# Performance work log

Hardware: AMD Instinct MI355X
Metric: run time of the kernel (lower is better)

Reference implementation:

```python
import jax, jax.numpy as jnp
import numpy as np

D = 128      # flattened state dim (n_dim)
T = 128      # time grid length
N = 32       # quadrature nodes per integral
H = 256      # func MLP hidden
HK = 64      # kernel MLP hidden
ITERS = 3    # IDESolver max_iterations


def setup_inputs() -> dict:
    key = jax.random.key(0)
    ks = jax.random.split(key, 6)
    z0 = jax.random.normal(ks[0], (1, D), jnp.float32)
    t = jnp.linspace(0.0, 1.0, T, dtype=jnp.float32)
    W1 = jax.random.normal(ks[1], (D, H), jnp.float32) / np.float32(np.sqrt(D))
    b1 = jnp.zeros((H,), jnp.float32)
    W2 = jax.random.normal(ks[2], (H, D), jnp.float32) / np.float32(np.sqrt(H))
    b2 = jnp.zeros((D,), jnp.float32)
    Wk1 = jax.random.normal(ks[3], (2, HK), jnp.float32) / np.float32(np.sqrt(2))
    bk1 = jnp.zeros((HK,), jnp.float32)
    # small kernel init keeps the Picard iteration stable
    Wk2 = jax.random.normal(ks[4], (HK, D * D), jnp.float32) * np.float32(0.01 / np.sqrt(HK))
    bk2 = jnp.zeros((D * D,), jnp.float32)
    return dict(z0=z0, t=t, W1=W1, b1=b1, W2=W2, b2=b2,
                Wk1=Wk1, bk1=bk1, Wk2=Wk2, bk2=bk2)


def _spline_coeffs(x, y):
    # natural cubic spline second derivatives M: tridiagonal system, natural BC
    n = x.shape[0]
    h = x[1:] - x[:-1]                       # [T-1]
    A = jnp.zeros((n, n), y.dtype).at[0, 0].set(1.0).at[n - 1, n - 1].set(1.0)
    idx = jnp.arange(1, n - 1)
    A = A.at[idx, idx - 1].set(h[:-1])
    A = A.at[idx, idx].set(2.0 * (h[:-1] + h[1:]))
    A = A.at[idx, idx + 1].set(h[1:])
    slope = (y[1:] - y[:-1]) / h[:, None]
    rhs = jnp.zeros_like(y).at[1:-1].set(6.0 * (slope[1:] - slope[:-1]))
    return jnp.linalg.solve(A, rhs)          # [T, D]


def _spline_eval(x, y, M, q):
    # evaluate spline at flat query points q [Q] -> [Q, D]
    qc = jnp.clip(q, x[0], x[-1])
    i = jnp.clip(jnp.searchsorted(x, qc, side='right') - 1, 0, x.shape[0] - 2)
    h = x[i + 1] - x[i]
    a = (x[i + 1] - qc) / h
    b = (qc - x[i]) / h
    return (a[:, None] * y[i] + b[:, None] * y[i + 1]
            + ((a ** 3 - a)[:, None] * M[i] + (b ** 3 - b)[:, None] * M[i + 1])
            * (h ** 2 / 6.0)[:, None])


def _F(y, W1, b1, W2, b2):
    return jnp.tanh(y @ W1 + b1) @ W2 + b2


def _K(ts, Wk1, bk1, Wk2, bk2):
    # ts [..., 2] -> kernel matrices [..., D, D]
    hden = jnp.tanh(ts @ Wk1 + bk1)
    return (hden @ Wk2 + bk2).reshape(ts.shape[:-1] + (D, D))


def reference(z0, t, W1, b1, W2, b2, Wk1, bk1, Wk2, bk2):
    y0 = z0.reshape(-1)                          # solver state: flattened z0 [D]
    u = jnp.linspace(0.0, 1.0, N, dtype=t.dtype) # unit quad nodes
    wq = jnp.ones((N,), t.dtype).at[0].set(0.5).at[-1].set(0.5)  # trapezoid
    mids = 0.5 * (t[:-1] + t[1:])
    xs = jnp.concatenate([t, mids])              # eval points [P = 2T-1]
    hstep = t[1:] - t[:-1]
    yg = jnp.broadcast_to(y0, (T, D))            # Picard initial guess y^(0)=y0
    for _ in range(ITERS):
        M = _spline_coeffs(t, yg)
        s = xs[:, None] * u[None, :]                              # [P, N], lb=0, ub=x
        ys = _spline_eval(t, yg, M, s.reshape(-1)).reshape(-1, N, D)
        fy = _F(ys, W1, b1, W2, b2)                               # [P, N, D]
        ts = jnp.stack([jnp.broadcast_to(xs[:, None], s.shape), s], -1)
        k = _K(ts, Wk1, bk1, Wk2, bk2)                            # [P, N, D, D]
        integ = jnp.einsum('pnij,pnj->pni', k, fy)
        g = jnp.einsum('pni,n->pi', integ, wq) * (xs / (N - 1))[:, None]  # [P, D]
        g_t, g_m = g[:T], g[T:]
        # Simpson (== RK4 for y-independent RHS) + cumulative integration
        inc = (hstep[:, None] / 6.0) * (g_t[:-1] + 4.0 * g_m + g_t[1:])
        yg = y0[None, :] + jnp.concatenate(
            [jnp.zeros((1, D), yg.dtype), jnp.cumsum(inc, axis=0)])
    return yg[:, None, :]                        # [T, 1, D] like solver.y.unsqueeze(1)
```

## Files before the change

kernel.cpp:

```cpp
#include <hip/hip_runtime.h>
#include <hip/hip_fp16.h>

#define D_  128
#define T_  128
#define P_  255
#define GSZ  32640

#define OFF_YGF   0
#define OFF_COEF  8192
#define OFF_AINV  8704
#define OFF_E     41472
#define OFF_HDW   563712
#define OFF_W1F   828912
#define OFF_W2F   845296
#define OFF_WTT   861680
#define OFF_S     1394160
#define OFF_G2    2459120
#define OFF_CTR   2491760

typedef _Float16 f16;
typedef _Float16 f16x4 __attribute__((ext_vector_type(4)));
typedef float f32x4 __attribute__((ext_vector_type(4)));

__device__ __forceinline__ float tanh_fast(float x) {
  float e = __expf(2.0f * x);
  return 1.0f - 2.0f / (e + 1.0f);
}

__device__ __forceinline__ f16x4 ldfrag(const f16* buf, int row, int kunits,
                                        int kk, int quad) {
  int u = row * kunits + ((kk * 4 + quad) ^ (row & 7));
  return *(const f16x4*)(buf + 4 * u);
}

__global__ __launch_bounds__(256) void k_setup(
    const float* __restrict__ z0, const float* __restrict__ tgrid,
    const float* __restrict__ W1, const float* __restrict__ W2,
    const float* __restrict__ Wk2, const float* __restrict__ bk2,
    __half* __restrict__ ygF, float* __restrict__ coef,
    float* __restrict__ Ainv, __half* __restrict__ W1F,
    __half* __restrict__ W2F, __half* __restrict__ WTC,
    unsigned* __restrict__ ctr) {
  __shared__ __align__(16) unsigned char smem[66560];
  int bid = blockIdx.x, tid = threadIdx.x;
  for (int idx = bid * 256 + tid; idx < 65 * 16384; idx += 256 * 256) {
    int c = idx >> 14, rem = idx & 16383;
    int i = rem >> 7, j = rem & 127;
    float v = (c < 64) ? Wk2[idx] : bk2[rem];
    int kc = c / 5;
    int kr = (c - kc * 5) * 128 + j;
    int kb = kr >> 6, kw = kr & 63;
    WTC[(((kc * 10 + kb) << 7) + i) * 64 + kw] = __float2half(v);
  }
  if (bid == 0) {
    for (int idx = tid; idx < 16384; idx += 256) {
      int l2 = (idx >> 2) & 63, blk = idx >> 8;
      int nt = blk >> 3, rr = l2 & 15;
      ygF[idx] = __float2half(z0[nt * 16 + rr]);
    }
  } else if (bid == 1) {
    for (int idx = tid; idx < 32768; idx += 256) {
      int j = idx & 3, l2 = (idx >> 2) & 63, blk = idx >> 8;
      int nt = blk >> 3, kk = blk & 7, rr = l2 & 15, qd = l2 >> 4;
      int c = nt * 16 + rr, d = kk * 16 + qd * 4 + j;
      W1F[idx] = __float2half(W1[d * 256 + c]);
    }
  } else if (bid == 2) {
    for (int idx = tid; idx < 32768; idx += 256) {
      int j = idx & 3, l2 = (idx >> 2) & 63, blk = idx >> 8;
      int nt = blk >> 4, kk = blk & 15, rr = l2 & 15, qd = l2 >> 4;
      int jcol = nt * 16 + rr, c = kk * 16 + qd * 4 + j;
      W2F[idx] = __float2half(W2[c * 128 + jcol]);
    }
  } else if (bid == 3) {
    if (tid == 0) *ctr = 0u;
  } else if (bid == 255) {
    float* dpL = (float*)smem;
    float* tl  = (float*)(smem + 65024);
    float* cpL = tl + 128;
    float* imL = cpL + 128;
    if (tid < 128) tl[tid] = tgrid[tid];
    __syncthreads();
    if (tid == 0) {
      cpL[0] = 0.0f;
      float cprev = 0.0f;
      for (int i = 1; i <= 126; ++i) {
        float hm = tl[i] - tl[i - 1], hi = tl[i + 1] - tl[i];
        float m = 2.0f * (hm + hi) - hm * cprev;
        float im = 1.0f / m;
        imL[i] = im;
        cprev = hi * im;
        cpL[i] = cprev;
      }
    }
    if (tid < 127) coef[256 + tid] = 1.0f / (tl[tid + 1] - tl[tid]);
    __syncthreads();
    if (tid < 128) {
      int d = tid;
      float dprev = (d == 0) ? 1.0f : 0.0f;
      dpL[d] = dprev;
      for (int i = 1; i <= 126; ++i) {
        float rhs = (i == d) ? 1.0f : 0.0f;
        float hm = tl[i] - tl[i - 1];
        dprev = (rhs - hm * dprev) * imL[i];
        dpL[i * 128 + d] = dprev;
      }
      float x = (d == 127) ? 1.0f : 0.0f;
      Ainv[127 * 128 + d] = x;
      for (int i = 126; i >= 0; --i) {
        x = dpL[i * 128 + d] - cpL[i] * x;
        Ainv[i * 128 + d] = x;
      }
    }
  }
}

__global__ __launch_bounds__(512) void k_fused(
    __half* __restrict__ EF, __half* __restrict__ HDW,
    const __half* __restrict__ ygF,
    const __half* __restrict__ W1F, const __half* __restrict__ W2F,
    const float* __restrict__ b1, const float* __restrict__ b2,
    __half* __restrict__ Sq, float* __restrict__ g,
    const float* __restrict__ tgrid, const float* __restrict__ Wk1,
    const float* __restrict__ bk1, const float* __restrict__ coef,
    const float* __restrict__ Ainv, int it) {
  __shared__ __align__(16) unsigned char smem[32768];
  __shared__ float tl[128], ihL[128];
  __shared__ float sn[32], an[32], bn[32], cA[32], cB[32];
  __shared__ int idn[32];
  f16* RA = (f16*)smem;
  f16* RB = (f16*)(smem + 8192);
  f16* RC = (f16*)(smem + 16384);
  int p = blockIdx.x, tid = threadIdx.x;
  int wv = tid >> 6, l = tid & 63, quad = l >> 4, r = l & 15;

  if (tid < 128) g[p * 128 + tid] = 0.0f;
  if (p == 0) {
    for (int z = tid; z < 8320; z += 512) {
      int kcS = z / 640, kr = z - kcS * 640;
      Sq[kcS * 163840 + 255 * 640 + kr] = __float2half(0.0f);
    }
  }

  if (it == 0) {
    if (tid < 128) tl[tid] = tgrid[tid];
    if (tid < 127) ihL[tid] = coef[256 + tid];
    __syncthreads();
    float xp = (p < T_) ? tl[p] : 0.5f * (tl[p - T_] + tl[p - T_ + 1]);
    if (tid < 32) {
      int n = tid;
      float u = (float)n * (1.0f / 31.0f);
      float q = xp * u;
      float qc = fminf(fmaxf(q, tl[0]), tl[127]);
      int i = (int)floorf(qc * 127.0f);
      i = max(0, min(126, i));
      while (i > 0 && qc < tl[i]) --i;
      while (i < 126 && qc >= tl[i + 1]) ++i;
      float h = tl[i + 1] - tl[i];
      float aa = (tl[i + 1] - qc) / h, bb = (qc - tl[i]) / h;
      sn[n] = q; idn[n] = i; an[n] = aa; bn[n] = bb;
      float h26 = h * h * (1.0f / 6.0f);
      cA[n] = (aa * aa * aa - aa) * h26;
      cB[n] = (bb * bb * bb - bb) * h26;
    }
    __syncthreads();
    #pragma unroll
    for (int pass = 0; pass < 8; ++pass) {
      int n = pass * 4 + (tid >> 7);
      int b = tid & 127;
      int i = idn[n];
      float Gi = 0.0f, Gi1 = 0.0f;
      if (b >= 2) {
        float w = 6.0f * ihL[b - 1];
        Gi  += Ainv[i * 128 + b - 1] * w;
        Gi1 += Ainv[(i + 1) * 128 + b - 1] * w;
      }
      if (b >= 1 && b <= 126) {
        float w = -6.0f * (ihL[b - 1] + ihL[b]);
        Gi  += Ainv[i * 128 + b] * w;
        Gi1 += Ainv[(i + 1) * 128 + b] * w;
      }
      if (b <= 125) {
        float w = 6.0f * ihL[b];
        Gi  += Ainv[i * 128 + b + 1] * w;
        Gi1 += Ainv[(i + 1) * 128 + b + 1] * w;
      }
      float v = cA[n] * Gi + cB[n] * Gi1;
      if (b == i) v += an[n];
      if (b == i + 1) v += bn[n];
      int mtE = n >> 4, rrE = n & 15;
      int kkE = b >> 4, qdE = (b >> 2) & 3, jE = b & 3;
      EF[p * 4096 + ((((mtE * 8 + kkE) * 64 + qdE * 16 + rrE)) << 2) + jE] =
          __float2half(v);
    }
    #pragma unroll
    for (int k = 0; k < 5; ++k) {
      int idx = k * 512 + tid;
      if (idx < 2080) {
        int c = idx >> 5, n = idx & 31;
        float wq = (n == 0 || n == 31) ? 0.5f : 1.0f;
        float v = (c < 64)
            ? wq * tanh_fast(fmaf(xp, Wk1[c], fmaf(sn[n], Wk1[64 + c], bk1[c])))
            : wq;
        HDW[p * 2080 + idx] = __float2half(v);
      }
    }
    __syncthreads();
  }

  uint2 pfh[2];
  {
    const uint2* sh_ = (const uint2*)(HDW + p * 2080);
    #pragma unroll
    for (int k = 0; k < 2; ++k) {
      int idx = k * 512 + tid;
      if (idx < 640) pfh[k] = (idx < 520) ? sh_[idx] : make_uint2(0u, 0u);
    }
  }
  const f16* efp = (const f16*)EF + p * 4096;
  for (int tt = wv; tt < 16; tt += 8) {
    int mt = tt >> 3, nt = tt & 7;
    f32x4 acc = {0.f, 0.f, 0.f, 0.f};
    #pragma unroll
    for (int kk = 0; kk < 8; ++kk) {
      f16x4 av = *(const f16x4*)(efp + (((mt * 8 + kk) * 64 + l) << 2));
      f16x4 bv = *(const f16x4*)((const f16*)ygF + (((nt * 8 + kk) * 64 + l) << 2));
      acc = __builtin_amdgcn_mfma_f32_16x16x16f16(av, bv, acc, 0, 0, 0);
    }
    int col = nt * 16 + r;
    #pragma unroll
    for (int i = 0; i < 4; ++i) {
      int row = mt * 16 + quad * 4 + i;
      RB[row * 128 + (col ^ ((row & 7) << 2))] = (f16)acc[i];
    }
  }
  __syncthreads();
  for (int tt = wv; tt < 32; tt += 8) {
    int mt = tt >> 4, nt = tt & 15;
    f32x4 acc = {0.f, 0.f, 0.f, 0.f};
    #pragma unroll
    for (int kk = 0; kk < 8; ++kk) {
      f16x4 av = ldfrag(RB, mt * 16 + r, 32, kk, quad);
      f16x4 bv = *(const f16x4*)((const f16*)W1F + (((nt * 8 + kk) * 64 + l) << 2));
      acc = __builtin_amdgcn_mfma_f32_16x16x16f16(av, bv, acc, 0, 0, 0);
    }
    int colg = nt * 16 + r;
    float bias = b1[colg];
    #pragma unroll
    for (int i = 0; i < 4; ++i) {
      int row = mt * 16 + quad * 4 + i;
      RC[row * 256 + (colg ^ ((row & 7) << 2))] = (f16)tanh_fast(acc[i] + bias);
    }
  }
  __syncthreads();
  {
    uint2* db = (uint2*)RB;
    #pragma unroll
    for (int k = 0; k < 2; ++k) {
      int idx = k * 512 + tid;
      if (idx < 640) {
        int row = idx >> 3, k4 = idx & 7;
        db[row * 8 + (k4 ^ (row & 7))] = pfh[k];
      }
    }
  }
  for (int tt = wv; tt < 16; tt += 8) {
    int mt = tt >> 3, nt = tt & 7;
    f32x4 acc = {0.f, 0.f, 0.f, 0.f};
    #pragma unroll
    for (int kk = 0; kk < 16; ++kk) {
      f16x4 av = ldfrag(RC, mt * 16 + r, 64, kk, quad);
      f16x4 bv = *(const f16x4*)((const f16*)W2F + (((nt * 16 + kk) * 64 + l) << 2));
      acc = __builtin_amdgcn_mfma_f32_16x16x16f16(av, bv, acc, 0, 0, 0);
    }
    int jg = nt * 16 + r;
    float bias = b2[jg];
    #pragma unroll
    for (int i = 0; i < 4; ++i) {
      int n = mt * 16 + quad * 4 + i;
      RA[jg * 32 + (n ^ ((jg & 7) << 2))] = (f16)(acc[i] + bias);
    }
  }
  __syncthreads();
  for (int tt = wv; tt < 40; tt += 8) {
    int mt = tt >> 3, nt = tt & 7;
    f32x4 acc = {0.f, 0.f, 0.f, 0.f};
    #pragma unroll
    for (int kk = 0; kk < 2; ++kk) {
      f16x4 av = ldfrag(RB, mt * 16 + r, 8, kk, quad);
      f16x4 bv = ldfrag(RA, nt * 16 + r, 8, kk, quad);
      acc = __builtin_amdgcn_mfma_f32_16x16x16f16(av, bv, acc, 0, 0, 0);
    }
    #pragma unroll
    for (int i = 0; i < 4; ++i) {
      int c = mt * 16 + quad * 4 + i;
      if (c < 65) {
        int col = nt * 16 + r;
        int kcS = c / 5;
        int kr = (c - kcS * 5) * 128 + col;
        Sq[kcS * 163840 + p * 640 + kr] = __float2half(acc[i]);
      }
    }
  }
}

__global__ __launch_bounds__(256) void k_gemmM(
    const __half* __restrict__ Sq, const __half* __restrict__ WTC,
    float* __restrict__ g, const float* __restrict__ t,
    const float* __restrict__ z0, __half* __restrict__ ygF,
    float* __restrict__ out, unsigned* __restrict__ ctr, int wout) {
  __shared__ __align__(16) unsigned char smem[65280];
  __shared__ unsigned lastFlag;
  uint2* Asw  = (uint2*)smem;
  uint2* Bsw0 = (uint2*)(smem + 20480);
  uint2* Bsw1 = (uint2*)(smem + 36864);
  int mt = blockIdx.x;
  int kc = blockIdx.y;
  int tid = threadIdx.x;
  int wv = tid >> 6, l = tid & 63, quad = l >> 4, r = l & 15;
  int p0 = mt * 16;
  int rowT = tid >> 4, u4lo = tid & 15;
  {
    const uint2* srcA = (const uint2*)(Sq + kc * 163840 + (p0 + rowT) * 640) + u4lo;
    #pragma unroll
    for (int pass = 0; pass < 10; ++pass) {
      int u4 = pass * 16 + u4lo;
      Asw[rowT * 160 + (u4 ^ (rowT & 7))] = srcA[pass * 16];
    }
  }
  const uint2* bbase = (const uint2*)WTC + kc * 10 * 2048;
  #pragma unroll
  for (int pass = 0; pass < 8; ++pass) {
    int idx = pass * 256 + tid;
    int row = idx >> 4, u4 = idx & 15;
    Bsw0[row * 16 + (u4 ^ (row & 7))] = bbase[idx];
  }
  __syncthreads();
  f32x4 acc0 = {0.f, 0.f, 0.f, 0.f}, acc1 = {0.f, 0.f, 0.f, 0.f};
  int n0 = wv * 32;
  const f16* Af = (const f16*)Asw;
  for (int kb = 0; kb < 10; ++kb) {
    const f16* Bf = (const f16*)((kb & 1) ? Bsw1 : Bsw0);
    uint2* nxtB = (kb & 1) ? Bsw0 : Bsw1;
    uint2 pf[8];
    if (kb < 9) {
      const uint2* srcN = bbase + (kb + 1) * 2048;
      #pragma unroll
      for (int pass = 0; pass < 8; ++pass) pf[pass] = srcN[pass * 256 + tid];
    }
    #pragma unroll
    for (int kk = 0; kk < 4; ++kk) {
      int kg4 = kb * 16 + kk * 4 + quad;
      f16x4 av = *(const f16x4*)(Af + 4 * (r * 160 + (kg4 ^ (r & 7))));
      int nr0 = n0 + r, nr1 = n0 + 16 + r;
      f16x4 b0 = *(const f16x4*)(Bf + 4 * (nr0 * 16 + ((kk * 4 + quad) ^ (nr0 & 7))));
      f16x4 b1 = *(const f16x4*)(Bf + 4 * (nr1 * 16 + ((kk * 4 + quad) ^ (nr1 & 7))));
      acc0 = __builtin_amdgcn_mfma_f32_16x16x16f16(av, b0, acc0, 0, 0, 0);
      acc1 = __builtin_amdgcn_mfma_f32_16x16x16f16(av, b1, acc1, 0, 0, 0);
    }
    if (kb < 9) {
      #pragma unroll
      for (int pass = 0; pass < 8; ++pass) {
        int idx = pass * 256 + tid;
        int row = idx >> 4, u4 = idx & 15;
        nxtB[row * 16 + (u4 ^ (row & 7))] = pf[pass];
      }
    }
    __syncthreads();
  }
  #pragma unroll
  for (int i = 0; i < 4; ++i) {
    int p = p0 + quad * 4 + i;
    if (p < 255) {
      atomicAdd(&g[p * 128 + n0 + r], acc0[i]);
      atomicAdd(&g[p * 128 + n0 + 16 + r], acc1[i]);
    }
  }
  __threadfence();
  if (tid == 0) {
    unsigned old = atomicAdd(ctr, 1u);
    lastFlag = (old == 207u) ? 1u : 0u;
    if (lastFlag) *ctr = 0u;
  }
  __syncthreads();
  if (!lastFlag) return;
  __threadfence();
  float* incL = (float*)smem;
  for (int idx = tid; idx < 127 * 128; idx += 256) {
    int k = idx >> 7, d = idx & 127;
    float tk = t[k], tk1 = t[k + 1];
    float h = tk1 - tk;
    float sct  = tk * (1.0f / 31.0f);
    float scm  = 0.5f * (tk + tk1) * (1.0f / 31.0f);
    float sct1 = tk1 * (1.0f / 31.0f);
    incL[idx] = h * (1.0f / 6.0f) *
        (g[k * 128 + d] * sct + 4.0f * g[(T_ + k) * 128 + d] * scm +
         g[(k + 1) * 128 + d] * sct1);
  }
  __syncthreads();
  if (tid < 128) {
    int d = tid, ntF = d >> 4, rrF = d & 15;
    float acc = z0[d];
    ygF[((ntF * 8) * 64 + rrF) << 2] = __float2half(acc);
    if (wout) out[d] = acc;
    #pragma unroll 4
    for (int k = 0; k < 127; ++k) {
      acc += incL[k * 128 + d];
      int kp = k + 1;
      int kkF = kp >> 4, qdF = (kp >> 2) & 3, jF = kp & 3;
      ygF[((((ntF * 8 + kkF) * 64 + qdF * 16 + rrF)) << 2) + jF] =
          __float2half(acc);
      if (wout) out[kp * 128 + d] = acc;
    }
  }
}

extern "C" void kernel_launch(void* const* d_in, const int* in_sizes, int n_in,
                              void* d_out, int out_size, void* d_ws, size_t ws_size,
                              hipStream_t stream) {
  const float* z0  = (const float*)d_in[0];
  const float* t   = (const float*)d_in[1];
  const float* W1  = (const float*)d_in[2];
  const float* b1  = (const float*)d_in[3];
  const float* W2  = (const float*)d_in[4];
  const float* b2  = (const float*)d_in[5];
  const float* Wk1 = (const float*)d_in[6];
  const float* bk1 = (const float*)d_in[7];
  const float* Wk2 = (const float*)d_in[8];
  const float* bk2 = (const float*)d_in[9];
  float* out = (float*)d_out;
  float* ws  = (float*)d_ws;

  __half*   ygF  = (__half*)(ws + OFF_YGF);
  float*    coef = ws + OFF_COEF;
  float*    Ainv = ws + OFF_AINV;
  __half*   EF   = (__half*)(ws + OFF_E);
  __half*   HDW  = (__half*)(ws + OFF_HDW);
  __half*   W1F  = (__half*)(ws + OFF_W1F);
  __half*   W2F  = (__half*)(ws + OFF_W2F);
  __half*   WTC  = (__half*)(ws + OFF_WTT);
  __half*   Sq   = (__half*)(ws + OFF_S);
  float*    g    = ws + OFF_G2;
  unsigned* ctr  = (unsigned*)(ws + OFF_CTR);

  k_setup<<<dim3(256), dim3(256), 0, stream>>>(z0, t, W1, W2, Wk2, bk2,
                                               ygF, coef, Ainv, W1F, W2F, WTC,
                                               ctr);
  for (int it = 0; it < 3; ++it) {
    k_fused<<<dim3(255), dim3(512), 0, stream>>>(EF, HDW, ygF, W1F, W2F,
                                                 b1, b2, Sq, g, t, Wk1, bk1,
                                                 coef, Ainv, it);
    k_gemmM<<<dim3(16, 13), dim3(256), 0, stream>>>(Sq, WTC, g, t, z0, ygF, out,
                                                    ctr, (it == 2) ? 1 : 0);
  }
}
```

Measured before the change: 167.4 us.

## Store GEMM operands in MFMA fragment order and load directly from global

The S matrix written by the fused kernel and the kernel weight matrix prepared in setup are now stored in the exact per-lane MFMA fragment layout. The M-GEMM kernel loads each fragment straight from global memory with one vector load per lane, with no shared-memory staging, double buffering or per-k-block barriers. This removes LDS traffic and synchronisation from the GEMM. The cost is that it relies on cache hits for the reused B operand across blocks and no longer explicitly overlaps loads with compute, and the fused kernel's scattered stores into the new layout may cost more.

```diff
diff --git a/kernel.cpp b/kernel.cpp
--- a/kernel.cpp
+++ b/kernel.cpp
@@ -13,7 +13,7 @@
 #define OFF_HDW   563712
 #define OFF_W1F   828912
 #define OFF_W2F   845296
-#define OFF_WTT   861680
+#define OFF_WF    861680
 #define OFF_S     1394160
 #define OFF_G2    2459120
 #define OFF_CTR   2491760
@@ -31,6 +31,14 @@
                                         int kk, int quad) {
   int u = row * kunits + ((kk * 4 + quad) ^ (row & 7));
   return *(const f16x4*)(buf + 4 * u);
+}
+
+__device__ __forceinline__ int AFidx(int kc, int p, int kr) {
+  int mtA = p >> 4, rA = p & 15;
+  int kb = kr >> 6, rem = kr & 63;
+  int kk = rem >> 4, quad = (rem >> 2) & 3, j = rem & 3;
+  int lane = quad * 16 + rA;
+  return kc * 163840 + ((((mtA * 10 + kb) * 4 + kk) * 64 + lane) << 2) + j;
 }
 
 __global__ __launch_bounds__(256) void k_setup(
@@ -39,7 +47,7 @@
     const float* __restrict__ Wk2, const float* __restrict__ bk2,
     __half* __restrict__ ygF, float* __restrict__ coef,
     float* __restrict__ Ainv, __half* __restrict__ W1F,
-    __half* __restrict__ W2F, __half* __restrict__ WTC,
+    __half* __restrict__ W2F, __half* __restrict__ WF,
     unsigned* __restrict__ ctr) {
   __shared__ __align__(16) unsigned char smem[66560];
   int bid = blockIdx.x, tid = threadIdx.x;
@@ -49,8 +57,11 @@
     float v = (c < 64) ? Wk2[idx] : bk2[rem];
     int kc = c / 5;
     int kr = (c - kc * 5) * 128 + j;
-    int kb = kr >> 6, kw = kr & 63;
-    WTC[(((kc * 10 + kb) << 7) + i) * 64 + kw] = __float2half(v);
+    int kb = kr >> 6, rem2 = kr & 63;
+    int kkf = rem2 >> 4, quadf = (rem2 >> 2) & 3, jf = rem2 & 3;
+    int lane = quadf * 16 + (i & 15), ntB = i >> 4;
+    WF[kc * 81920 + ((((kb * 4 + kkf) * 8 + ntB) * 64 + lane) << 2) + jf] =
+        __float2half(v);
   }
   if (bid == 0) {
     for (int idx = tid; idx < 16384; idx += 256) {
@@ -120,7 +131,7 @@
     const __half* __restrict__ ygF,
     const __half* __restrict__ W1F, const __half* __restrict__ W2F,
     const float* __restrict__ b1, const float* __restrict__ b2,
-    __half* __restrict__ Sq, float* __restrict__ g,
+    __half* __restrict__ AF, float* __restrict__ g,
     const float* __restrict__ tgrid, const float* __restrict__ Wk1,
     const float* __restrict__ bk1, const float* __restrict__ coef,
     const float* __restrict__ Ainv, int it) {
@@ -138,7 +149,7 @@
   if (p == 0) {
     for (int z = tid; z < 8320; z += 512) {
       int kcS = z / 640, kr = z - kcS * 640;
-      Sq[kcS * 163840 + 255 * 640 + kr] = __float2half(0.0f);
+      AF[AFidx(kcS, 255, kr)] = __float2half(0.0f);
     }
   }
 
@@ -298,76 +309,39 @@
         int col = nt * 16 + r;
         int kcS = c / 5;
         int kr = (c - kcS * 5) * 128 + col;
-        Sq[kcS * 163840 + p * 640 + kr] = __float2half(acc[i]);
+        AF[AFidx(kcS, p, kr)] = __float2half(acc[i]);
       }
     }
   }
 }
 
 __global__ __launch_bounds__(256) void k_gemmM(
-    const __half* __restrict__ Sq, const __half* __restrict__ WTC,
+    const __half* __restrict__ AF, const __half* __restrict__ WF,
     float* __restrict__ g, const float* __restrict__ t,
     const float* __restrict__ z0, __half* __restrict__ ygF,
     float* __restrict__ out, unsigned* __restrict__ ctr, int wout) {
-  __shared__ __align__(16) unsigned char smem[65280];
+  __shared__ float incL[127 * 128];
   __shared__ unsigned lastFlag;
-  uint2* Asw  = (uint2*)smem;
-  uint2* Bsw0 = (uint2*)(smem + 20480);
-  uint2* Bsw1 = (uint2*)(smem + 36864);
   int mt = blockIdx.x;
   int kc = blockIdx.y;
   int tid = threadIdx.x;
   int wv = tid >> 6, l = tid & 63, quad = l >> 4, r = l & 15;
   int p0 = mt * 16;
-  int rowT = tid >> 4, u4lo = tid & 15;
-  {
-    const uint2* srcA = (const uint2*)(Sq + kc * 163840 + (p0 + rowT) * 640) + u4lo;
-    #pragma unroll
-    for (int pass = 0; pass < 10; ++pass) {
-      int u4 = pass * 16 + u4lo;
-      Asw[rowT * 160 + (u4 ^ (rowT & 7))] = srcA[pass * 16];
-    }
-  }
-  const uint2* bbase = (const uint2*)WTC + kc * 10 * 2048;
-  #pragma unroll
-  for (int pass = 0; pass < 8; ++pass) {
-    int idx = pass * 256 + tid;
-    int row = idx >> 4, u4 = idx & 15;
-    Bsw0[row * 16 + (u4 ^ (row & 7))] = bbase[idx];
-  }
-  __syncthreads();
+  const f16* abase = (const f16*)AF + kc * 163840 + ((mt * 10) << 10);
+  const f16* bbase = (const f16*)WF + kc * 81920;
   f32x4 acc0 = {0.f, 0.f, 0.f, 0.f}, acc1 = {0.f, 0.f, 0.f, 0.f};
-  int n0 = wv * 32;
-  const f16* Af = (const f16*)Asw;
+  int nt0 = wv * 2, nt1 = wv * 2 + 1;
   for (int kb = 0; kb < 10; ++kb) {
-    const f16* Bf = (const f16*)((kb & 1) ? Bsw1 : Bsw0);
-    uint2* nxtB = (kb & 1) ? Bsw0 : Bsw1;
-    uint2 pf[8];
-    if (kb < 9) {
-      const uint2* srcN = bbase + (kb + 1) * 2048;
-      #pragma unroll
-      for (int pass = 0; pass < 8; ++pass) pf[pass] = srcN[pass * 256 + tid];
-    }
     #pragma unroll
     for (int kk = 0; kk < 4; ++kk) {
-      int kg4 = kb * 16 + kk * 4 + quad;
-      f16x4 av = *(const f16x4*)(Af + 4 * (r * 160 + (kg4 ^ (r & 7))));
-      int nr0 = n0 + r, nr1 = n0 + 16 + r;
-      f16x4 b0 = *(const f16x4*)(Bf + 4 * (nr0 * 16 + ((kk * 4 + quad) ^ (nr0 & 7))));
-      f16x4 b1 = *(const f16x4*)(Bf + 4 * (nr1 * 16 + ((kk * 4 + quad) ^ (nr1 & 7))));
+      f16x4 av = *(const f16x4*)(abase + (((kb * 4 + kk) * 64 + l) << 2));
+      f16x4 b0 = *(const f16x4*)(bbase + ((((kb * 4 + kk) * 8 + nt0) * 64 + l) << 2));
+      f16x4 b1 = *(const f16x4*)(bbase + ((((kb * 4 + kk) * 8 + nt1) * 64 + l) << 2));
       acc0 = __builtin_amdgcn_mfma_f32_16x16x16f16(av, b0, acc0, 0, 0, 0);
       acc1 = __builtin_amdgcn_mfma_f32_16x16x16f16(av, b1, acc1, 0, 0, 0);
     }
-    if (kb < 9) {
-      #pragma unroll
-      for (int pass = 0; pass < 8; ++pass) {
-        int idx = pass * 256 + tid;
-        int row = idx >> 4, u4 = idx & 15;
-        nxtB[row * 16 + (u4 ^ (row & 7))] = pf[pass];
-      }
-    }
-    __syncthreads();
-  }
+  }
+  int n0 = wv * 32;
   #pragma unroll
   for (int i = 0; i < 4; ++i) {
     int p = p0 + quad * 4 + i;
@@ -385,7 +359,6 @@
   __syncthreads();
   if (!lastFlag) return;
   __threadfence();
-  float* incL = (float*)smem;
   for (int idx = tid; idx < 127 * 128; idx += 256) {
     int k = idx >> 7, d = idx & 127;
     float tk = t[k], tk1 = t[k + 1];
@@ -438,19 +411,19 @@
   __half*   HDW  = (__half*)(ws + OFF_HDW);
   __half*   W1F  = (__half*)(ws + OFF_W1F);
   __half*   W2F  = (__half*)(ws + OFF_W2F);
-  __half*   WTC  = (__half*)(ws + OFF_WTT);
-  __half*   Sq   = (__half*)(ws + OFF_S);
+  __half*   WF   = (__half*)(ws + OFF_WF);
+  __half*   AF   = (__half*)(ws + OFF_S);
   float*    g    = ws + OFF_G2;
   unsigned* ctr  = (unsigned*)(ws + OFF_CTR);
 
   k_setup<<<dim3(256), dim3(256), 0, stream>>>(z0, t, W1, W2, Wk2, bk2,
-                                               ygF, coef, Ainv, W1F, W2F, WTC,
+                                               ygF, coef, Ainv, W1F, W2F, WF,
                                                ctr);
   for (int it = 0; it < 3; ++it) {
     k_fused<<<dim3(255), dim3(512), 0, stream>>>(EF, HDW, ygF, W1F, W2F,
-                                                 b1, b2, Sq, g, t, Wk1, bk1,
+                                                 b1, b2, AF, g, t, Wk1, bk1,
                                                  coef, Ainv, it);
-    k_gemmM<<<dim3(16, 13), dim3(256), 0, stream>>>(Sq, WTC, g, t, z0, ygF, out,
+    k_gemmM<<<dim3(16, 13), dim3(256), 0, stream>>>(AF, WF, g, t, z0, ygF, out,
                                                     ctr, (it == 2) ? 1 : 0);
   }
 }
```

Result: slower. 184.8 us (+10.4%).
